# Kernel tuning notes

Measured on AMD Instinct MI355X. Metric: run time of the kernel, lower is better.

Reference implementation:

```python
import jax, jax.numpy as jnp
import numpy as np

EPS = 0.5
MIN_PTS = 10


def setup_inputs() -> dict:
    key = jax.random.key(0)
    point_features = jax.random.normal(key, (4, 8192, 16), dtype=jnp.float32)
    return {"point_features": point_features}


def reference(point_features) -> jnp.ndarray:
    # torch.cdist(x, x): pairwise Euclidean distances, shape [B, N, N]
    x = point_features
    sq = jnp.sum(x * x, axis=-1)                      # [B, N]
    # squared distances via ||a||^2 + ||b||^2 - 2 a.b
    d2 = sq[:, :, None] + sq[:, None, :] - 2.0 * jnp.einsum('bnd,bmd->bnm', x, x)
    dist = jnp.sqrt(jnp.maximum(d2, 0.0))             # [B, N, N]
    # neighbors = 1 where dist < eps (includes self, dist==0)
    neighbor_count = jnp.sum(dist < EPS, axis=2)      # [B, N] int
    # final_clusters starts at 0; points with too few neighbors marked -1 (noise)
    final_clusters = jnp.where(neighbor_count < MIN_PTS, -1, 0).astype(jnp.int32)
    return final_clusters
```

## Files before the change

### kernel.cpp

```cpp
#include <hip/hip_runtime.h>


constexpr int Np = 8192;
constexpr int Bb = 4;
constexpr int MIN_PTS = 10;
constexpr float EPS2_4 = 0.0625f;
constexpr int JS = 16;
constexpr int JW = Np / JS;
constexpr int ICH = 256;
constexpr int RF = 4;
constexpr int NT = JW / 16;

typedef __bf16 bf16x8 __attribute__((ext_vector_type(8)));
typedef float  f32x4  __attribute__((ext_vector_type(4)));

#define GLOBAL_LOAD_LDS16(gptr, lptr)                                          \
    __builtin_amdgcn_global_load_lds(                                          \
        (const __attribute__((address_space(1))) void*)(gptr),                 \
        (__attribute__((address_space(3))) void*)(lptr), 16, 0, 0)

__global__ __launch_bounds__(256)
void dbscan_prep(const float* __restrict__ x, __bf16* __restrict__ aug,
                 int* __restrict__ out) {
    const int p = blockIdx.x * 256 + threadIdx.x;
    const float4* src = (const float4*)(x + (size_t)p * 16);
    float4 v0 = src[0], v1 = src[1], v2 = src[2], v3 = src[3];
    float vv[16];
    vv[0]=v0.x; vv[1]=v0.y; vv[2]=v0.z; vv[3]=v0.w;
    vv[4]=v1.x; vv[5]=v1.y; vv[6]=v1.z; vv[7]=v1.w;
    vv[8]=v2.x; vv[9]=v2.y; vv[10]=v2.z; vv[11]=v2.w;
    vv[12]=v3.x; vv[13]=v3.y; vv[14]=v3.z; vv[15]=v3.w;
    float s = 0.f;
#pragma unroll
    for (int k = 0; k < 16; k++) s = fmaf(vv[k], vv[k], s);
    const float g = 0.5f * s - EPS2_4;
    bf16x8 h0, h1, h2;
#pragma unroll
    for (int k = 0; k < 8; k++) { h0[k] = (__bf16)vv[k]; h1[k] = (__bf16)vv[k+8]; }
    h2[0] = (__bf16)1.0f; h2[1] = (__bf16)(-g);
#pragma unroll
    for (int k = 2; k < 8; k++) h2[k] = (__bf16)0.0f;

    const int b   = p >> 13;
    const int pin = p & 8191;
    const int js  = pin >> 9;
    const int tl  = (pin >> 4) & 31;
    const int m   = pin & 15;
    bf16x8* dst = (bf16x8*)aug + (((size_t)(b * 16 + js) * 32 + tl) * 48 + m);
    dst[0]  = h0;
    dst[16] = h1;
    dst[32] = h2;
    out[p] = 0;
}

__global__ __launch_bounds__(256, 6)
void dbscan_count(const __bf16* __restrict__ aug, int* __restrict__ out) {
    const int lane = threadIdx.x & 63;
    const int w    = threadIdx.x >> 6;
    const int m    = lane & 15;
    const int q    = lane >> 4;
    const int blk  = blockIdx.x;
    const int b    = blk >> 9;
    const int ic   = (blk >> 4) & 31;
    const int js   = blk & 15;
    const int ibase = ic * ICH;

    __shared__ __bf16 ldsB[NT * 48 * 8];

    {
        const __bf16* src = aug + ((size_t)(b * 16 + js) * 32) * 48 * 8;
#pragma unroll
        for (int it = 0; it < 6; it++) {
            const int c = threadIdx.x + it * 256;
            GLOBAL_LOAD_LDS16(src + (size_t)c * 8, ldsB + (size_t)c * 8);
        }
    }

    bf16x8 af[RF];
    const int qa = (q < 3) ? q : 2;
#pragma unroll
    for (int f = 0; f < RF; f++) {
        const int rowbase = ibase + w * 64 + f * 16;
        const int jsA = rowbase >> 9;
        const int tlA = (rowbase >> 4) & 31;
        const __bf16* ap = aug +
            (((size_t)(b * 16 + jsA) * 32 + tlA) * 48 + qa * 16 + m) * 8;
        bf16x8 a = *(const bf16x8*)ap;
        if (q == 2) { __bf16 t = a[0]; a[0] = a[1]; a[1] = t; }
        if (q == 3) {
#pragma unroll
            for (int k = 0; k < 8; k++) a[k] = (__bf16)0.0f;
        }
        af[f] = a;
    }

    __syncthreads();

    const __bf16* bptr = ldsB + (q < 3 ? (q * 16 + m) * 8 : 0);

    const f32x4 zacc = {0.f, 0.f, 0.f, 0.f};
    int cnt[16];
#pragma unroll
    for (int i = 0; i < 16; i++) cnt[i] = 0;

    bf16x8 bc = *(const bf16x8*)bptr;
#pragma unroll 2
    for (int t = 0; t < NT; t++) {
        const int tn = (t + 1) & (NT - 1);
        bf16x8 bn = *(const bf16x8*)(bptr + tn * 48 * 8);
#pragma unroll
        for (int f = 0; f < RF; f++) {
            f32x4 acc = __builtin_amdgcn_mfma_f32_16x16x32_bf16(af[f], bc, zacc, 0, 0, 0);
            cnt[f*4+0] += __float_as_int(acc[0]) >> 31;
            cnt[f*4+1] += __float_as_int(acc[1]) >> 31;
            cnt[f*4+2] += __float_as_int(acc[2]) >> 31;
            cnt[f*4+3] += __float_as_int(acc[3]) >> 31;
        }
        bc = bn;
    }

#pragma unroll
    for (int i = 0; i < 16; i++) {
        int v = cnt[i];
        v += __shfl_xor(v, 1);
        v += __shfl_xor(v, 2);
        v += __shfl_xor(v, 4);
        v += __shfl_xor(v, 8);
        cnt[i] = v;
    }
    if (m == 0) {
        int* ob = out + (size_t)b * Np + ibase + w * 64;
#pragma unroll
        for (int f = 0; f < RF; f++)
#pragma unroll
            for (int r = 0; r < 4; r++)
                atomicAdd(&ob[f*16 + q*4 + r], JW + cnt[f*4+r]);
    }
}

__global__ __launch_bounds__(256)
void dbscan_classify(int* __restrict__ out) {
    const int p = blockIdx.x * 256 + threadIdx.x;
    out[p] = (out[p] < MIN_PTS) ? -1 : 0;
}

extern "C" void kernel_launch(void* const* d_in, const int* in_sizes, int n_in,
                              void* d_out, int out_size, void* d_ws, size_t ws_size,
                              hipStream_t stream) {
    const float* x = (const float*)d_in[0];
    int* out = (int*)d_out;
    __bf16* aug = (__bf16*)d_ws;

    dbscan_prep<<<dim3(Bb * Np / 256), dim3(256), 0, stream>>>(x, aug, out);
    dbscan_count<<<dim3(Bb * 32 * JS), dim3(256), 0, stream>>>(aug, out);
    dbscan_classify<<<dim3(Bb * Np / 256), dim3(256), 0, stream>>>(out);
}
```

Measured before the change: 75.97 us.

## Give each block full j range, double-buffer per-wave LDS, fuse classify

Each block now owns 64 rows and scans all 8192 columns, with the four waves splitting the column range and each wave streaming 128-column slabs into its own double-buffered LDS region through async global-to-LDS loads. Partial counts are reduced across waves in shared memory and the block writes the final -1/0 label directly. This removes the atomics, the output zeroing in prep, and the separate classify launch. In exchange there are only 512 blocks, far fewer than before, and the occupancy hint drops from 6 to 2, so latency hiding relies on the explicit prefetch pipeline.

```diff
diff --git a/kernel.cpp b/kernel.cpp
--- a/kernel.cpp
+++ b/kernel.cpp
@@ -5,11 +5,14 @@
 constexpr int Bb = 4;
 constexpr int MIN_PTS = 10;
 constexpr float EPS2_4 = 0.0625f;
-constexpr int JS = 16;
-constexpr int JW = Np / JS;
-constexpr int ICH = 256;
+constexpr int ICH = 64;
 constexpr int RF = 4;
-constexpr int NT = JW / 16;
+constexpr int NWAVE = 4;
+constexpr int JPW = Np / NWAVE;
+constexpr int SW = 128;
+constexpr int NSW = JPW / SW;
+constexpr int NT = SW / 16;
+constexpr int SWB = SW * 24;
 
 typedef __bf16 bf16x8 __attribute__((ext_vector_type(8)));
 typedef float  f32x4  __attribute__((ext_vector_type(4)));
@@ -20,8 +23,7 @@
         (__attribute__((address_space(3))) void*)(lptr), 16, 0, 0)
 
 __global__ __launch_bounds__(256)
-void dbscan_prep(const float* __restrict__ x, __bf16* __restrict__ aug,
-                 int* __restrict__ out) {
+void dbscan_prep(const float* __restrict__ x, __bf16* __restrict__ aug) {
     const int p = blockIdx.x * 256 + threadIdx.x;
     const float4* src = (const float4*)(x + (size_t)p * 16);
     float4 v0 = src[0], v1 = src[1], v2 = src[2], v3 = src[3];
@@ -50,37 +52,42 @@
     dst[0]  = h0;
     dst[16] = h1;
     dst[32] = h2;
-    out[p] = 0;
 }
 
-__global__ __launch_bounds__(256, 6)
+__global__ __launch_bounds__(256, 2)
 void dbscan_count(const __bf16* __restrict__ aug, int* __restrict__ out) {
     const int lane = threadIdx.x & 63;
     const int w    = threadIdx.x >> 6;
     const int m    = lane & 15;
     const int q    = lane >> 4;
     const int blk  = blockIdx.x;
-    const int b    = blk >> 9;
-    const int ic   = (blk >> 4) & 31;
-    const int js   = blk & 15;
+    const int b    = blk >> 7;
+    const int ic   = blk & 127;
     const int ibase = ic * ICH;
 
-    __shared__ __bf16 ldsB[NT * 48 * 8];
+    __shared__ __align__(16) __bf16 ldsB[NWAVE * 2 * SWB];
+    __shared__ int partial[NWAVE][ICH];
 
-    {
-        const __bf16* src = aug + ((size_t)(b * 16 + js) * 32) * 48 * 8;
+    auto stage = [&](int buf, int sw) {
+        const int jj0 = w * JPW + sw * SW;
+        const int js  = jj0 >> 9;
+        const int tl0 = (jj0 >> 4) & 31;
+        const __bf16* src = aug + (((size_t)(b * 16 + js) * 32 + tl0) * 48) * 8;
+        __bf16* dst = ldsB + (size_t)(w * 2 + buf) * SWB;
 #pragma unroll
-        for (int it = 0; it < 6; it++) {
-            const int c = threadIdx.x + it * 256;
-            GLOBAL_LOAD_LDS16(src + (size_t)c * 8, ldsB + (size_t)c * 8);
+        for (int it = 0; it < 6; ++it) {
+            const int c = it * 64 + lane;
+            GLOBAL_LOAD_LDS16(src + (size_t)c * 8, dst + (size_t)c * 8);
         }
-    }
+    };
+
+    stage(0, 0);
 
     bf16x8 af[RF];
     const int qa = (q < 3) ? q : 2;
 #pragma unroll
     for (int f = 0; f < RF; f++) {
-        const int rowbase = ibase + w * 64 + f * 16;
+        const int rowbase = ibase + f * 16;
         const int jsA = rowbase >> 9;
         const int tlA = (rowbase >> 4) & 31;
         const __bf16* ap = aug +
@@ -94,29 +101,36 @@
         af[f] = a;
     }
 
-    __syncthreads();
-
-    const __bf16* bptr = ldsB + (q < 3 ? (q * 16 + m) * 8 : 0);
-
     const f32x4 zacc = {0.f, 0.f, 0.f, 0.f};
     int cnt[16];
 #pragma unroll
     for (int i = 0; i < 16; i++) cnt[i] = 0;
 
-    bf16x8 bc = *(const bf16x8*)bptr;
-#pragma unroll 2
-    for (int t = 0; t < NT; t++) {
-        const int tn = (t + 1) & (NT - 1);
-        bf16x8 bn = *(const bf16x8*)(bptr + tn * 48 * 8);
+    const int boff = (q < 3 ? (q * 16 + m) * 8 : 0);
+
+    int buf = 0;
+    for (int sw = 0; sw < NSW; ++sw) {
+        if (sw + 1 < NSW) {
+            stage(buf ^ 1, sw + 1);
+            asm volatile("s_waitcnt vmcnt(6)" ::: "memory");
+        } else {
+            asm volatile("s_waitcnt vmcnt(0)" ::: "memory");
+        }
+        __builtin_amdgcn_sched_barrier(0);
+        const __bf16* base = ldsB + (size_t)(w * 2 + buf) * SWB + boff;
 #pragma unroll
-        for (int f = 0; f < RF; f++) {
-            f32x4 acc = __builtin_amdgcn_mfma_f32_16x16x32_bf16(af[f], bc, zacc, 0, 0, 0);
-            cnt[f*4+0] += __float_as_int(acc[0]) >> 31;
-            cnt[f*4+1] += __float_as_int(acc[1]) >> 31;
-            cnt[f*4+2] += __float_as_int(acc[2]) >> 31;
-            cnt[f*4+3] += __float_as_int(acc[3]) >> 31;
+        for (int t = 0; t < NT; ++t) {
+            bf16x8 bc = *(const bf16x8*)(base + t * 48 * 8);
+#pragma unroll
+            for (int f = 0; f < RF; f++) {
+                f32x4 acc = __builtin_amdgcn_mfma_f32_16x16x32_bf16(af[f], bc, zacc, 0, 0, 0);
+                cnt[f*4+0] += __float_as_int(acc[0]) >> 31;
+                cnt[f*4+1] += __float_as_int(acc[1]) >> 31;
+                cnt[f*4+2] += __float_as_int(acc[2]) >> 31;
+                cnt[f*4+3] += __float_as_int(acc[3]) >> 31;
+            }
         }
-        bc = bn;
+        buf ^= 1;
     }
 
 #pragma unroll
@@ -129,19 +143,21 @@
         cnt[i] = v;
     }
     if (m == 0) {
-        int* ob = out + (size_t)b * Np + ibase + w * 64;
 #pragma unroll
         for (int f = 0; f < RF; f++)
 #pragma unroll
             for (int r = 0; r < 4; r++)
-                atomicAdd(&ob[f*16 + q*4 + r], JW + cnt[f*4+r]);
+                partial[w][f * 16 + q * 4 + r] = cnt[f*4 + r];
     }
-}
+    __syncthreads();
 
-__global__ __launch_bounds__(256)
-void dbscan_classify(int* __restrict__ out) {
-    const int p = blockIdx.x * 256 + threadIdx.x;
-    out[p] = (out[p] < MIN_PTS) ? -1 : 0;
+    if (threadIdx.x < ICH) {
+        const int row = threadIdx.x;
+        const int s = partial[0][row] + partial[1][row] +
+                      partial[2][row] + partial[3][row];
+        const int count = Np + s;
+        out[(size_t)b * Np + ibase + row] = (count < MIN_PTS) ? -1 : 0;
+    }
 }
 
 extern "C" void kernel_launch(void* const* d_in, const int* in_sizes, int n_in,
@@ -151,7 +167,6 @@
     int* out = (int*)d_out;
     __bf16* aug = (__bf16*)d_ws;
 
-    dbscan_prep<<<dim3(Bb * Np / 256), dim3(256), 0, stream>>>(x, aug, out);
-    dbscan_count<<<dim3(Bb * 32 * JS), dim3(256), 0, stream>>>(aug, out);
-    dbscan_classify<<<dim3(Bb * Np / 256), dim3(256), 0, stream>>>(out);
+    dbscan_prep<<<dim3(Bb * Np / 256), dim3(256), 0, stream>>>(x, aug);
+    dbscan_count<<<dim3(Bb * (Np / ICH)), dim3(256), 0, stream>>>(aug, out);
 }
```

Measured after the change: 80.30 us. +5.7%, slower.
